# Kernel tuning notes

Measured on AMD Instinct MI355X. Metric: run time of the kernel, lower is better.

Reference implementation:

```python
import jax, jax.numpy as jnp
import numpy as np

N_HEADS = 16
ROPE_BASE = 10000.0


def rope_angles(seq_len, head_dim):
    # freq[n, i] = n / base^(2i/head_dim), shape [N, head_dim//2]
    inv_freq = 1.0 / (ROPE_BASE ** (jnp.arange(0, head_dim, 2, dtype=jnp.float32) / head_dim))
    return jnp.arange(seq_len, dtype=jnp.float32)[:, None] * inv_freq[None, :]


def apply_rope(t, ang):
    # t: [B, h, N, D], ang: [N, D//2]; rotate half-split pairs
    cos = jnp.cos(ang)[None, None]  # [1,1,N,D//2]
    sin = jnp.sin(ang)[None, None]
    d2 = t.shape[-1] // 2
    t1, t2 = t[..., :d2], t[..., d2:]
    return jnp.concatenate([t1 * cos - t2 * sin, t1 * sin + t2 * cos], axis=-1)


def setup_inputs() -> dict:
    key = jax.random.key(0)
    k1, k2, k3 = jax.random.split(key, 3)
    B, N, D = 2, 2048, 2048
    x = jax.random.normal(k1, (B, N, D), dtype=jnp.float32)
    w_qkv = jax.random.normal(k2, (3 * D, D), dtype=jnp.float32) * (D ** -0.5)
    w_proj = jax.random.normal(k3, (D, D), dtype=jnp.float32) * (D ** -0.5)
    b_proj = jnp.zeros((D,), dtype=jnp.float32)
    return {"x": x, "w_qkv": w_qkv, "w_proj": w_proj, "b_proj": b_proj}


def reference(x, w_qkv, w_proj, b_proj):
    B, N, D = x.shape
    h = N_HEADS
    hd = D // h

    qkv = jnp.einsum('bnd,ed->bne', x, w_qkv)  # [B, N, 3D]
    q, k, v = jnp.split(qkv, 3, axis=-1)

    def to_heads(t):  # [B,N,D] -> [B,h,N,hd]
        return t.reshape(B, N, h, hd).transpose(0, 2, 1, 3)

    q, k, v = to_heads(q), to_heads(k), to_heads(v)

    ang = rope_angles(N, hd)
    q = apply_rope(q, ang)
    k = apply_rope(k, ang)

    scale = 1.0 / jnp.sqrt(jnp.asarray(hd, dtype=x.dtype))
    scores = jnp.einsum('bhqd,bhkd->bhqk', q, k) * scale  # [B,h,N,N]
    attn = jax.nn.softmax(scores, axis=-1)
    out = jnp.einsum('bhqk,bhkd->bhqd', attn, v)  # [B,h,N,hd]

    out = out.transpose(0, 2, 1, 3).reshape(B, N, D)
    return jnp.einsum('bnd,ed->bne', out, w_proj) + b_proj
```

## Files before the change

### kernel.cpp

```cpp
#include <hip/hip_runtime.h>
#include <hip/hip_bf16.h>

using bf16 = __hip_bfloat16;
typedef __attribute__((ext_vector_type(8))) short bf16x8;
typedef __attribute__((ext_vector_type(4))) float f32x4;
typedef __attribute__((ext_vector_type(16))) float f32x16;
typedef __attribute__((ext_vector_type(4))) unsigned int u32x4;

constexpr int Bz  = 2;
constexpr int SEQ = 2048;
constexpr int DM  = 2048;
constexpr int H   = 16;
constexpr int HD  = 128;
constexpr long MROWS = (long)Bz * SEQ;
constexpr int EQ  = 3 * DM;
constexpr float QSCALE_L2E = 0.12751743427795914f;

__device__ __forceinline__ float bf2f(bf16 x) { return __bfloat162float(x); }
__device__ __forceinline__ bf16  f2bf(float x) { return __float2bfloat16(x); }

__device__ __forceinline__ float fexp2(float x) {
  float r;
  asm("v_exp_f32 %0, %1" : "=v"(r) : "v"(x));
  return r;
}

template <int N>
__device__ __forceinline__ void waitvm() {
  asm volatile("s_waitcnt vmcnt(%0)" ::"n"(N) : "memory");
}

__device__ __forceinline__ void gl_lds16(const void* g, void* l) {
  __builtin_amdgcn_global_load_lds(
      (const __attribute__((address_space(1))) unsigned int*)g,
      (__attribute__((address_space(3))) unsigned int*)l, 16, 0, 0);
}

__global__ void f32_to_bf16(const float* __restrict__ in, bf16* __restrict__ out, long n) {
  long i = ((long)blockIdx.x * blockDim.x + threadIdx.x) * 4;
  if (i >= n) return;
  float4 v = *(const float4*)(in + i);
  bf16 tmp[4] = {f2bf(v.x), f2bf(v.y), f2bf(v.z), f2bf(v.w)};
  *(uint2*)(out + i) = *(uint2*)tmp;
}

__global__ void rope_table(float* __restrict__ ct, float* __restrict__ st) {
  int idx = blockIdx.x * 256 + threadIdx.x;
  if (idx >= SEQ * 64) return;
  int j = idx & 63, n = idx >> 6;
  double inv = exp(-(double)j / 64.0 * 9.210340371976184);
  double a = (double)n * inv;
  ct[idx] = (float)cos(a);
  st[idx] = (float)sin(a);
}

template <int KTOT, int BN, int NBP, int OUT_BF16>
__global__ __launch_bounds__(512) void gemm128(const bf16* __restrict__ A,
                                               const bf16* __restrict__ Bm,
                                               void* __restrict__ Cv,
                                               const float* __restrict__ bias,
                                               int M, int Nn) {
  constexpr int NT = KTOT / 64;
  __shared__ alignas(16) bf16 lsA[2][128 * 64];
  __shared__ alignas(16) bf16 lsB[2][BN * 64];

  const int nwg = gridDim.x;
  const int f = blockIdx.x;
  const int wg = (f & 7) * (nwg >> 3) + (f >> 3);
  const int nbm = M >> 7;
  const long am0 = (long)(wg % nbm) * 128;
  const long bn0 = (long)(wg / nbm) * BN;

  const int tid = threadIdx.x;
  const int wv = tid >> 6, ln = tid & 63;
  const int wm = wv & 1, wn = wv >> 1;
  const int fr = ln & 15, kq = ln >> 4;
  const int sr8 = ln >> 3;
  const int ss  = ln & 7;

  f32x4 acc[4][2 * NBP] = {};
  bf16x8 af[8];
  bf16x8 bq[4];

  auto stageA = [&](int buf, int t) {
#pragma unroll
    for (int ld = 0; ld < 2; ++ld) {
      const int r = ld * 64 + wv * 8 + sr8;
      const int sl = ss ^ (r & 7);
      gl_lds16(A + (am0 + r) * KTOT + t * 64 + sl * 8, &lsA[buf][(ld * 64 + wv * 8) * 64]);
    }
  };
  auto stageB = [&](int buf, int t, int bp) {
#pragma unroll
    for (int ld = 0; ld < 2; ++ld) {
      const int r = bp * 128 + ld * 64 + wv * 8 + sr8;
      const int sl = ss ^ (r & 7);
      gl_lds16(Bm + (bn0 + r) * KTOT + t * 64 + sl * 8,
               &lsB[buf][(bp * 128 + ld * 64 + wv * 8) * 64]);
    }
  };

  stageA(0, 0);
#pragma unroll
  for (int bp = 0; bp < NBP; ++bp) stageB(0, 0, bp);
  waitvm<0>();
  __builtin_amdgcn_s_barrier();

#pragma unroll 2
  for (int t = 0; t < NT; ++t) {
    const int cur = t & 1;
    const bool pre = (t + 1 < NT);

#pragma unroll
    for (int bp = 0; bp < NBP; ++bp) {
      if (bp == 0) {
#pragma unroll
        for (int i = 0; i < 4; ++i)
#pragma unroll
          for (int ks = 0; ks < 2; ++ks) {
            const int row = (wm + 2 * i) * 16 + fr;
            const int sl = (ks * 4 + kq) ^ (row & 7);
            af[i * 2 + ks] = *(const bf16x8*)((const char*)&lsA[cur][0] + row * 128 + sl * 16);
          }
      }
#pragma unroll
      for (int jj = 0; jj < 2; ++jj)
#pragma unroll
        for (int ks = 0; ks < 2; ++ks) {
          const int row = (wn + 4 * (2 * bp + jj)) * 16 + fr;
          const int sl = (ks * 4 + kq) ^ (row & 7);
          bq[jj * 2 + ks] = *(const bf16x8*)((const char*)&lsB[cur][0] + row * 128 + sl * 16);
        }

      if (pre) {
        if (bp == 0) {
          stageA(cur ^ 1, t + 1);
          stageB(cur ^ 1, t + 1, 0);
          waitvm<2 * NBP>();
        } else if (bp == NBP - 1) {
          stageB(cur ^ 1, t + 1, bp);
          waitvm<2 * (NBP - 1)>();
        } else {
          stageB(cur ^ 1, t + 1, bp);
          waitvm<2 * NBP>();
        }
      } else {
        if (bp == 0) waitvm<(NBP > 2) ? 2 : 0>();
        else waitvm<0>();
      }
      __builtin_amdgcn_s_barrier();

      __builtin_amdgcn_s_setprio(1);
#pragma unroll
      for (int i = 0; i < 4; ++i)
#pragma unroll
        for (int jj = 0; jj < 2; ++jj)
#pragma unroll
          for (int ks = 0; ks < 2; ++ks)
            acc[i][2 * bp + jj] = __builtin_amdgcn_mfma_f32_16x16x32_bf16(
                af[i * 2 + ks], bq[jj * 2 + ks], acc[i][2 * bp + jj], 0, 0, 0);
      __builtin_amdgcn_s_setprio(0);
    }
  }

#pragma unroll
  for (int i = 0; i < 4; ++i) {
    const long row0 = am0 + (wm + 2 * i) * 16 + kq * 4;
#pragma unroll
    for (int j = 0; j < 2 * NBP; ++j) {
      const long col = bn0 + (wn + 4 * j) * 16 + fr;
      const float bv = bias ? bias[col] : 0.f;
#pragma unroll
      for (int q = 0; q < 4; ++q) {
        const float v = acc[i][j][q] + bv;
        if (OUT_BF16) ((bf16*)Cv)[(row0 + q) * Nn + col] = f2bf(v);
        else          ((float*)Cv)[(row0 + q) * Nn + col] = v;
      }
    }
  }
}

__global__ void rope_reshape(const bf16* __restrict__ qkv, const float* __restrict__ ct,
                             const float* __restrict__ st, bf16* __restrict__ q_r,
                             bf16* __restrict__ k_r) {
  long idx = (long)blockIdx.x * 256 + threadIdx.x;
  int j = idx & 63;
  int h = (idx >> 6) & 15;
  int n = (idx >> 10) & 2047;
  int b = (int)(idx >> 21);
  long row = (long)b * SEQ + n;
  float c = ct[n * 64 + j], s = st[n * 64 + j];
  long qoff = row * EQ + h * 128 + j;
  float q1 = bf2f(qkv[qoff]),        q2 = bf2f(qkv[qoff + 64]);
  float k1 = bf2f(qkv[qoff + 2048]), k2 = bf2f(qkv[qoff + 2048 + 64]);
  long obase = ((long)(b * 16 + h) * SEQ + n) * HD + j;
  q_r[obase]      = f2bf((q1 * c - q2 * s) * QSCALE_L2E);
  q_r[obase + 64] = f2bf((q1 * s + q2 * c) * QSCALE_L2E);
  k_r[obase]      = f2bf(k1 * c - k2 * s);
  k_r[obase + 64] = f2bf(k1 * s + k2 * c);
}

__global__ __launch_bounds__(256) void v_transpose(const bf16* __restrict__ qkv,
                                                   bf16* __restrict__ v_t) {
  __shared__ bf16 tile[64][65];
  int bh = blockIdx.z;
  int b = bh >> 4, h = bh & 15;
  int n0 = blockIdx.y * 64, d0 = blockIdx.x * 64;
  int t = threadIdx.x;
#pragma unroll
  for (int p = 0; p < 16; ++p) {
    int e = p * 256 + t;
    int dn = e & 63, nn = e >> 6;
    tile[nn][dn] = qkv[(long)(b * SEQ + n0 + nn) * EQ + 2 * DM + h * 128 + d0 + dn];
  }
  __syncthreads();
#pragma unroll
  for (int p = 0; p < 16; ++p) {
    int e = p * 256 + t;
    int nn = e & 63, dd = e >> 6;
    v_t[((long)bh * HD + d0 + dd) * SEQ + n0 + nn] = tile[nn][dd];
  }
}

__global__ __launch_bounds__(256, 2) void attn_fwd(const bf16* __restrict__ q_r,
                                                   const bf16* __restrict__ k_r,
                                                   const bf16* __restrict__ v_t,
                                                   bf16* __restrict__ ao) {
  __shared__ alignas(16) char lds[65536];

  const int flat = blockIdx.y * gridDim.x + blockIdx.x;
  const int bh = (flat & 7) * 4 + ((flat >> 3) >> 4);
  const int qt = (flat >> 3) & 15;
  const int b = bh >> 4, h = bh & 15;

  const int wv = threadIdx.x >> 6, ln = threadIdx.x & 63;
  const int lh = ln >> 5;
  const int lq = ln & 31;
  const int q0 = qt * 128 + wv * 32;

  bf16x8 aq[8];
  {
    const char* qbase = (const char*)(q_r + ((long)bh * SEQ + q0 + lq) * HD);
#pragma unroll
    for (int ks = 0; ks < 8; ++ks)
      aq[ks] = *(const bf16x8*)(qbase + ks * 32 + lh * 16);
  }

  f32x16 oacc[4] = {};
  float mrow = -1e30f, lsum = 0.f;

  auto stage = [&](int buf, int t) {
    char* kb = lds + buf * 16384;
    char* vb = lds + 32768 + buf * 16384;
#pragma unroll
    for (int cc = 0; cc < 8; ++cc) {
      const int chunk = wv * 8 + cc;
      if (chunk < 16) {
        const int r = chunk * 4 + (ln >> 4);
        const char* src = (const char*)k_r + ((long)bh * SEQ + t * 64 + r) * 256 +
                          (((ln & 15) ^ (r & 15)) << 4);
        gl_lds16(src, kb + chunk * 1024);
      } else {
        const int c2 = chunk - 16;
        const int r = c2 * 8 + (ln >> 3);
        const char* src = (const char*)v_t + ((long)bh * HD + r) * (SEQ * 2) + t * 128 +
                          (((ln & 7) ^ (r & 7)) << 4);
        gl_lds16(src, vb + c2 * 1024);
      }
    }
  };

  stage(0, 0);
  __syncthreads();

  for (int t = 0; t < SEQ / 64; ++t) {
    const int cur = t & 1;
    if (t + 1 < SEQ / 64) stage(cur ^ 1, t + 1);
    const char* kb = lds + cur * 16384;
    const char* vb = lds + 32768 + cur * 16384;

    f32x16 sacc[2] = {};
    __builtin_amdgcn_s_setprio(1);
#pragma unroll
    for (int kvs = 0; kvs < 2; ++kvs) {
      const int kv = kvs * 32 + lq;
#pragma unroll
      for (int ks = 0; ks < 8; ++ks) {
        bf16x8 kf = *(const bf16x8*)(kb + kv * 256 + ((((ks << 1) | lh) ^ (kv & 15)) << 4));
        sacc[kvs] = __builtin_amdgcn_mfma_f32_32x32x16_bf16(kf, aq[ks], sacc[kvs], 0, 0, 0);
      }
    }
    __builtin_amdgcn_s_setprio(0);

    float mx = sacc[0][0];
#pragma unroll
    for (int r = 1; r < 16; ++r) mx = fmaxf(mx, sacc[0][r]);
#pragma unroll
    for (int r = 0; r < 16; ++r) mx = fmaxf(mx, sacc[1][r]);
    mx = fmaxf(mx, __shfl_xor(mx, 32, 64));
    const float mn = fmaxf(mrow, mx);
    const float scale = fexp2(mrow - mn);
    mrow = mn;
    float psum = 0.f;
#pragma unroll
    for (int k2 = 0; k2 < 2; ++k2)
#pragma unroll
      for (int r = 0; r < 16; ++r) {
        const float pv = fexp2(sacc[k2][r] - mn);
        sacc[k2][r] = pv;
        psum += pv;
      }
    psum += __shfl_xor(psum, 32, 64);
    lsum = lsum * scale + psum;
#pragma unroll
    for (int dt = 0; dt < 4; ++dt) oacc[dt] *= scale;

    bf16x8 pfrag[4];
#pragma unroll
    for (int k2 = 0; k2 < 2; ++k2) {
      unsigned int pk[8];
#pragma unroll
      for (int i = 0; i < 8; ++i) {
        unsigned int lo = __bfloat16_as_ushort(f2bf(sacc[k2][2 * i]));
        unsigned int hi = __bfloat16_as_ushort(f2bf(sacc[k2][2 * i + 1]));
        pk[i] = lo | (hi << 16);
      }
#pragma unroll
      for (int fb = 0; fb < 2; ++fb) {
        const unsigned int a0 = pk[fb * 4 + 0], a1 = pk[fb * 4 + 1];
        const unsigned int b0 = pk[fb * 4 + 2], b1 = pk[fb * 4 + 3];
        const unsigned int sb0 = __shfl_xor(b0, 32, 64);
        const unsigned int sb1 = __shfl_xor(b1, 32, 64);
        const unsigned int sa0 = __shfl_xor(a0, 32, 64);
        const unsigned int sa1 = __shfl_xor(a1, 32, 64);
        u32x4 wvec;
        wvec.x = lh ? sb0 : a0;
        wvec.y = lh ? sb1 : a1;
        wvec.z = lh ? b0 : sa0;
        wvec.w = lh ? b1 : sa1;
        pfrag[k2 * 2 + fb] = __builtin_bit_cast(bf16x8, wvec);
      }
    }

    __builtin_amdgcn_s_setprio(1);
#pragma unroll
    for (int dt = 0; dt < 4; ++dt) {
      const int d = dt * 32 + lq;
#pragma unroll
      for (int kk = 0; kk < 4; ++kk) {
        bf16x8 vf = *(const bf16x8*)(vb + d * 128 + ((((kk << 1) | lh) ^ (d & 7)) << 4));
        oacc[dt] = __builtin_amdgcn_mfma_f32_32x32x16_bf16(vf, pfrag[kk], oacc[dt], 0, 0, 0);
      }
    }
    __builtin_amdgcn_s_setprio(0);
    __syncthreads();
  }

  const float inv = 1.0f / lsum;
  bf16* ob = (bf16*)lds;
  const int qloc = wv * 32 + lq;
#pragma unroll
  for (int dt = 0; dt < 4; ++dt)
#pragma unroll
    for (int r = 0; r < 16; ++r) {
      const int d = dt * 32 + (r & 3) + 8 * (r >> 2) + 4 * lh;
      ob[qloc * 132 + d] = f2bf(oacc[dt][r] * inv);
    }
#pragma unroll
  for (int it = 0; it < 8; ++it) {
    const int c = it * 64 + ln;
    const int qq = c >> 4, dc = c & 15;
    const char* srcp = (const char*)ob + (wv * 32 + qq) * 264 + dc * 16;
    uint2 v0 = *(const uint2*)srcp;
    uint2 v1 = *(const uint2*)(srcp + 8);
    uint4 outv;
    outv.x = v0.x; outv.y = v0.y; outv.z = v1.x; outv.w = v1.y;
    *(uint4*)((char*)(ao + ((long)b * SEQ + qt * 128 + wv * 32 + qq) * DM + h * 128) + dc * 16) = outv;
  }
}

extern "C" void kernel_launch(void* const* d_in, const int* in_sizes, int n_in,
                              void* d_out, int out_size, void* d_ws, size_t ws_size,
                              hipStream_t stream) {
  const float* x      = (const float*)d_in[0];
  const float* w_qkv  = (const float*)d_in[1];
  const float* w_proj = (const float*)d_in[2];
  const float* b_proj = (const float*)d_in[3];

  char* ws = (char*)d_ws;
  size_t off = 0;
  auto alloc = [&](size_t bytes) {
    void* p = ws + off;
    off += (bytes + 255) & ~(size_t)255;
    return p;
  };
  bf16* xb     = (bf16*)alloc((size_t)MROWS * DM * 2);
  bf16* wqkvb  = (bf16*)alloc((size_t)EQ * DM * 2);
  bf16* wprojb = (bf16*)alloc((size_t)DM * DM * 2);
  bf16* qkvb   = (bf16*)alloc((size_t)MROWS * EQ * 2);
  bf16* q_r    = (bf16*)alloc((size_t)Bz * H * SEQ * HD * 2);
  bf16* k_r    = (bf16*)alloc((size_t)Bz * H * SEQ * HD * 2);
  bf16* v_t    = (bf16*)alloc((size_t)Bz * H * SEQ * HD * 2);
  bf16* aob    = (bf16*)alloc((size_t)MROWS * DM * 2);
  float* ct    = (float*)alloc((size_t)SEQ * 64 * 4);
  float* st    = (float*)alloc((size_t)SEQ * 64 * 4);

  {
    long n = MROWS * DM;
    f32_to_bf16<<<(int)((n / 4 + 255) / 256), 256, 0, stream>>>(x, xb, n);
  }
  {
    long n = (long)EQ * DM;
    f32_to_bf16<<<(int)((n / 4 + 255) / 256), 256, 0, stream>>>(w_qkv, wqkvb, n);
  }
  {
    long n = (long)DM * DM;
    f32_to_bf16<<<(int)((n / 4 + 255) / 256), 256, 0, stream>>>(w_proj, wprojb, n);
  }
  rope_table<<<(SEQ * 64) / 256, 256, 0, stream>>>(ct, st);

  gemm128<2048, 384, 3, 1><<<(int)(MROWS / 128) * (EQ / 384), 512, 0, stream>>>(
      xb, wqkvb, qkvb, nullptr, (int)MROWS, EQ);

  rope_reshape<<<(int)((long)Bz * SEQ * H * 64 / 256), 256, 0, stream>>>(qkvb, ct, st, q_r, k_r);
  v_transpose<<<dim3(HD / 64, SEQ / 64, Bz * H), 256, 0, stream>>>(qkvb, v_t);

  attn_fwd<<<dim3(16, Bz * H), 256, 0, stream>>>(q_r, k_r, v_t, aob);

  gemm128<2048, 256, 2, 0><<<(int)(MROWS / 128) * (DM / 256), 512, 0, stream>>>(
      aob, wprojb, d_out, b_proj, (int)MROWS, DM);
}
```

Before: 292.8 us.

## Vectorize rope/transpose, enlarge attention tiles, lazy softmax rescale, simplify GEMM pipeline

Rope and V-transpose now move data with 16-byte vector loads and stores instead of scalar accesses. The attention kernel goes to 512-thread blocks covering 256 queries each, so each K/V tile staged in LDS serves twice as many queries. The online softmax now rescales the running max and accumulators only when the new max exceeds the old one by more than 8 in the log2 domain. The GEMM main loop switches to issuing all next-tile prefetches up front with one wait and barrier per K step, replacing the interleaved per-subtile waits. These changes target memory inefficiency and per-tile overhead, at the cost of more LDS and registers per attention block and less overlap inside the GEMM.

```diff
diff --git a/kernel.cpp b/kernel.cpp
--- a/kernel.cpp
+++ b/kernel.cpp
@@ -18,6 +18,9 @@
 
 __device__ __forceinline__ float bf2f(bf16 x) { return __bfloat162float(x); }
 __device__ __forceinline__ bf16  f2bf(float x) { return __float2bfloat16(x); }
+__device__ __forceinline__ float rawbf(short u) {
+  return __uint_as_float(((unsigned int)(unsigned short)u) << 16);
+}
 
 __device__ __forceinline__ float fexp2(float x) {
   float r;
@@ -79,8 +82,6 @@
   const int ss  = ln & 7;
 
   f32x4 acc[4][2 * NBP] = {};
-  bf16x8 af[8];
-  bf16x8 bq[4];
 
   auto stageA = [&](int buf, int t) {
 #pragma unroll
@@ -106,23 +107,27 @@
   waitvm<0>();
   __builtin_amdgcn_s_barrier();
 
-#pragma unroll 2
   for (int t = 0; t < NT; ++t) {
     const int cur = t & 1;
-    const bool pre = (t + 1 < NT);
+    if (t + 1 < NT) {
+      stageA(cur ^ 1, t + 1);
+#pragma unroll
+      for (int bp = 0; bp < NBP; ++bp) stageB(cur ^ 1, t + 1, bp);
+    }
+
+    bf16x8 af[8];
+#pragma unroll
+    for (int i = 0; i < 4; ++i)
+#pragma unroll
+      for (int ks = 0; ks < 2; ++ks) {
+        const int row = (wm + 2 * i) * 16 + fr;
+        const int sl = (ks * 4 + kq) ^ (row & 7);
+        af[i * 2 + ks] = *(const bf16x8*)((const char*)&lsA[cur][0] + row * 128 + sl * 16);
+      }
 
 #pragma unroll
     for (int bp = 0; bp < NBP; ++bp) {
-      if (bp == 0) {
-#pragma unroll
-        for (int i = 0; i < 4; ++i)
-#pragma unroll
-          for (int ks = 0; ks < 2; ++ks) {
-            const int row = (wm + 2 * i) * 16 + fr;
-            const int sl = (ks * 4 + kq) ^ (row & 7);
-            af[i * 2 + ks] = *(const bf16x8*)((const char*)&lsA[cur][0] + row * 128 + sl * 16);
-          }
-      }
+      bf16x8 bq[4];
 #pragma unroll
       for (int jj = 0; jj < 2; ++jj)
 #pragma unroll
@@ -131,25 +136,6 @@
           const int sl = (ks * 4 + kq) ^ (row & 7);
           bq[jj * 2 + ks] = *(const bf16x8*)((const char*)&lsB[cur][0] + row * 128 + sl * 16);
         }
-
-      if (pre) {
-        if (bp == 0) {
-          stageA(cur ^ 1, t + 1);
-          stageB(cur ^ 1, t + 1, 0);
-          waitvm<2 * NBP>();
-        } else if (bp == NBP - 1) {
-          stageB(cur ^ 1, t + 1, bp);
-          waitvm<2 * (NBP - 1)>();
-        } else {
-          stageB(cur ^ 1, t + 1, bp);
-          waitvm<2 * NBP>();
-        }
-      } else {
-        if (bp == 0) waitvm<(NBP > 2) ? 2 : 0>();
-        else waitvm<0>();
-      }
-      __builtin_amdgcn_s_barrier();
-
       __builtin_amdgcn_s_setprio(1);
 #pragma unroll
       for (int i = 0; i < 4; ++i)
@@ -161,6 +147,9 @@
                 af[i * 2 + ks], bq[jj * 2 + ks], acc[i][2 * bp + jj], 0, 0, 0);
       __builtin_amdgcn_s_setprio(0);
     }
+
+    waitvm<0>();
+    __builtin_amdgcn_s_barrier();
   }
 
 #pragma unroll
@@ -184,59 +173,82 @@
                              const float* __restrict__ st, bf16* __restrict__ q_r,
                              bf16* __restrict__ k_r) {
   long idx = (long)blockIdx.x * 256 + threadIdx.x;
-  int j = idx & 63;
-  int h = (idx >> 6) & 15;
-  int n = (idx >> 10) & 2047;
-  int b = (int)(idx >> 21);
+  int j8 = (idx & 7) * 8;
+  int h = (idx >> 3) & 15;
+  int n = (idx >> 7) & 2047;
+  int b = (int)(idx >> 18);
   long row = (long)b * SEQ + n;
-  float c = ct[n * 64 + j], s = st[n * 64 + j];
-  long qoff = row * EQ + h * 128 + j;
-  float q1 = bf2f(qkv[qoff]),        q2 = bf2f(qkv[qoff + 64]);
-  float k1 = bf2f(qkv[qoff + 2048]), k2 = bf2f(qkv[qoff + 2048 + 64]);
-  long obase = ((long)(b * 16 + h) * SEQ + n) * HD + j;
-  q_r[obase]      = f2bf((q1 * c - q2 * s) * QSCALE_L2E);
-  q_r[obase + 64] = f2bf((q1 * s + q2 * c) * QSCALE_L2E);
-  k_r[obase]      = f2bf(k1 * c - k2 * s);
-  k_r[obase + 64] = f2bf(k1 * s + k2 * c);
+  long qoff = row * EQ + h * 128 + j8;
+  bf16x8 q1v = *(const bf16x8*)(qkv + qoff);
+  bf16x8 q2v = *(const bf16x8*)(qkv + qoff + 64);
+  bf16x8 k1v = *(const bf16x8*)(qkv + qoff + 2048);
+  bf16x8 k2v = *(const bf16x8*)(qkv + qoff + 2048 + 64);
+  float4 ca = *(const float4*)(ct + n * 64 + j8);
+  float4 cb = *(const float4*)(ct + n * 64 + j8 + 4);
+  float4 sa = *(const float4*)(st + n * 64 + j8);
+  float4 sb = *(const float4*)(st + n * 64 + j8 + 4);
+  float c[8] = {ca.x, ca.y, ca.z, ca.w, cb.x, cb.y, cb.z, cb.w};
+  float s[8] = {sa.x, sa.y, sa.z, sa.w, sb.x, sb.y, sb.z, sb.w};
+  bf16x8 oq1, oq2, ok1, ok2;
+#pragma unroll
+  for (int m = 0; m < 8; ++m) {
+    float q1 = rawbf(q1v[m]), q2 = rawbf(q2v[m]);
+    float k1 = rawbf(k1v[m]), k2 = rawbf(k2v[m]);
+    oq1[m] = (short)__bfloat16_as_ushort(f2bf((q1 * c[m] - q2 * s[m]) * QSCALE_L2E));
+    oq2[m] = (short)__bfloat16_as_ushort(f2bf((q1 * s[m] + q2 * c[m]) * QSCALE_L2E));
+    ok1[m] = (short)__bfloat16_as_ushort(f2bf(k1 * c[m] - k2 * s[m]));
+    ok2[m] = (short)__bfloat16_as_ushort(f2bf(k1 * s[m] + k2 * c[m]));
+  }
+  long obase = ((long)(b * 16 + h) * SEQ + n) * HD + j8;
+  *(bf16x8*)(q_r + obase)      = oq1;
+  *(bf16x8*)(q_r + obase + 64) = oq2;
+  *(bf16x8*)(k_r + obase)      = ok1;
+  *(bf16x8*)(k_r + obase + 64) = ok2;
 }
 
 __global__ __launch_bounds__(256) void v_transpose(const bf16* __restrict__ qkv,
                                                    bf16* __restrict__ v_t) {
-  __shared__ bf16 tile[64][65];
+  __shared__ bf16 tile[64][72];
   int bh = blockIdx.z;
   int b = bh >> 4, h = bh & 15;
   int n0 = blockIdx.y * 64, d0 = blockIdx.x * 64;
   int t = threadIdx.x;
 #pragma unroll
-  for (int p = 0; p < 16; ++p) {
-    int e = p * 256 + t;
-    int dn = e & 63, nn = e >> 6;
-    tile[nn][dn] = qkv[(long)(b * SEQ + n0 + nn) * EQ + 2 * DM + h * 128 + d0 + dn];
+  for (int it = 0; it < 2; ++it) {
+    int e = it * 256 + t;
+    int nn = e >> 3, dn8 = (e & 7) * 8;
+    bf16x8 v = *(const bf16x8*)(qkv + (long)(b * SEQ + n0 + nn) * EQ + 2 * DM + h * 128 + d0 + dn8);
+#pragma unroll
+    for (int m = 0; m < 8; ++m) tile[nn][dn8 + m] = __ushort_as_bfloat16((unsigned short)v[m]);
   }
   __syncthreads();
 #pragma unroll
-  for (int p = 0; p < 16; ++p) {
-    int e = p * 256 + t;
-    int nn = e & 63, dd = e >> 6;
-    v_t[((long)bh * HD + d0 + dd) * SEQ + n0 + nn] = tile[nn][dd];
-  }
-}
-
-__global__ __launch_bounds__(256, 2) void attn_fwd(const bf16* __restrict__ q_r,
+  for (int it = 0; it < 2; ++it) {
+    int e = it * 256 + t;
+    int dd = e >> 3, nn8 = (e & 7) * 8;
+    bf16x8 o;
+#pragma unroll
+    for (int m = 0; m < 8; ++m)
+      o[m] = (short)__bfloat16_as_ushort(tile[nn8 + m][dd]);
+    *(bf16x8*)(v_t + ((long)bh * HD + d0 + dd) * SEQ + n0 + nn8) = o;
+  }
+}
+
+__global__ __launch_bounds__(512, 2) void attn_fwd(const bf16* __restrict__ q_r,
                                                    const bf16* __restrict__ k_r,
                                                    const bf16* __restrict__ v_t,
                                                    bf16* __restrict__ ao) {
-  __shared__ alignas(16) char lds[65536];
-
-  const int flat = blockIdx.y * gridDim.x + blockIdx.x;
-  const int bh = (flat & 7) * 4 + ((flat >> 3) >> 4);
-  const int qt = (flat >> 3) & 15;
+  __shared__ alignas(16) char lds[69632];
+
+  const int flat = blockIdx.x;
+  const int bh = (flat & 7) * 4 + (flat >> 6);
+  const int qt = (flat >> 3) & 7;
   const int b = bh >> 4, h = bh & 15;
 
   const int wv = threadIdx.x >> 6, ln = threadIdx.x & 63;
   const int lh = ln >> 5;
   const int lq = ln & 31;
-  const int q0 = qt * 128 + wv * 32;
+  const int q0 = qt * 256 + wv * 32;
 
   bf16x8 aq[8];
   {
@@ -253,8 +265,8 @@
     char* kb = lds + buf * 16384;
     char* vb = lds + 32768 + buf * 16384;
 #pragma unroll
-    for (int cc = 0; cc < 8; ++cc) {
-      const int chunk = wv * 8 + cc;
+    for (int cc = 0; cc < 4; ++cc) {
+      const int chunk = wv * 4 + cc;
       if (chunk < 16) {
         const int r = chunk * 4 + (ln >> 4);
         const char* src = (const char*)k_r + ((long)bh * SEQ + t * 64 + r) * 256 +
@@ -298,22 +310,26 @@
 #pragma unroll
     for (int r = 0; r < 16; ++r) mx = fmaxf(mx, sacc[1][r]);
     mx = fmaxf(mx, __shfl_xor(mx, 32, 64));
-    const float mn = fmaxf(mrow, mx);
-    const float scale = fexp2(mrow - mn);
-    mrow = mn;
+
+    if (!__all(mx - mrow <= 8.0f)) {
+      const float mn = fmaxf(mrow, mx);
+      const float scale = fexp2(mrow - mn);
+      mrow = mn;
+      lsum *= scale;
+#pragma unroll
+      for (int dt = 0; dt < 4; ++dt) oacc[dt] *= scale;
+    }
     float psum = 0.f;
 #pragma unroll
     for (int k2 = 0; k2 < 2; ++k2)
 #pragma unroll
       for (int r = 0; r < 16; ++r) {
-        const float pv = fexp2(sacc[k2][r] - mn);
+        const float pv = fexp2(sacc[k2][r] - mrow);
         sacc[k2][r] = pv;
         psum += pv;
       }
     psum += __shfl_xor(psum, 32, 64);
-    lsum = lsum * scale + psum;
-#pragma unroll
-    for (int dt = 0; dt < 4; ++dt) oacc[dt] *= scale;
+    lsum += psum;
 
     bf16x8 pfrag[4];
 #pragma unroll
@@ -375,7 +391,7 @@
     uint2 v1 = *(const uint2*)(srcp + 8);
     uint4 outv;
     outv.x = v0.x; outv.y = v0.y; outv.z = v1.x; outv.w = v1.y;
-    *(uint4*)((char*)(ao + ((long)b * SEQ + qt * 128 + wv * 32 + qq) * DM + h * 128) + dc * 16) = outv;
+    *(uint4*)((char*)(ao + ((long)b * SEQ + qt * 256 + wv * 32 + qq) * DM + h * 128) + dc * 16) = outv;
   }
 }
 
@@ -422,10 +438,10 @@
   gemm128<2048, 384, 3, 1><<<(int)(MROWS / 128) * (EQ / 384), 512, 0, stream>>>(
       xb, wqkvb, qkvb, nullptr, (int)MROWS, EQ);
 
-  rope_reshape<<<(int)((long)Bz * SEQ * H * 64 / 256), 256, 0, stream>>>(qkvb, ct, st, q_r, k_r);
+  rope_reshape<<<(int)((long)Bz * SEQ * H * 8 / 256), 256, 0, stream>>>(qkvb, ct, st, q_r, k_r);
   v_transpose<<<dim3(HD / 64, SEQ / 64, Bz * H), 256, 0, stream>>>(qkvb, v_t);
 
-  attn_fwd<<<dim3(16, Bz * H), 256, 0, stream>>>(q_r, k_r, v_t, aob);
+  attn_fwd<<<256, 512, 0, stream>>>(q_r, k_r, v_t, aob);
 
   gemm128<2048, 256, 2, 0><<<(int)(MROWS / 128) * (DM / 256), 512, 0, stream>>>(
       aob, wprojb, d_out, b_proj, (int)MROWS, DM);
```

New measurement: 312.9 us. 1.07x slower.

## Fuse RoPE and V transpose into QKV GEMM epilogue, enlarge attention tiles, lazy rescale

Applied to the files above, without the earlier changes.

The QKV GEMM epilogue now stages its tile through shared memory and writes rotated, scaled Q and K plus transposed V directly. This removes the intermediate qkv buffer and the separate rope_reshape and v_transpose kernels. The attention kernel moves to 512 threads per block with 256 query rows per block, halving K/V loads per wave. Online softmax now skips the rescale unless the running max grows by more than 8 (log2 domain), which cuts exp and multiply work but lets unnormalized values grow, so precision could suffer.

```diff
diff --git a/kernel.cpp b/kernel.cpp
--- a/kernel.cpp
+++ b/kernel.cpp
@@ -54,15 +54,23 @@
   st[idx] = (float)sin(a);
 }
 
-template <int KTOT, int BN, int NBP, int OUT_BF16>
+template <int KTOT, int BN, int NBP, int FUSE>
 __global__ __launch_bounds__(512) void gemm128(const bf16* __restrict__ A,
                                                const bf16* __restrict__ Bm,
                                                void* __restrict__ Cv,
                                                const float* __restrict__ bias,
+                                               bf16* __restrict__ q_r,
+                                               bf16* __restrict__ k_r,
+                                               bf16* __restrict__ v_t,
+                                               const float* __restrict__ ct,
+                                               const float* __restrict__ st,
                                                int M, int Nn) {
   constexpr int NT = KTOT / 64;
-  __shared__ alignas(16) bf16 lsA[2][128 * 64];
-  __shared__ alignas(16) bf16 lsB[2][BN * 64];
+  constexpr int ASZ = 128 * 64;
+  constexpr int BSZ = BN * 64;
+  __shared__ alignas(16) char smem[2 * ASZ * 2 + 2 * BSZ * 2];
+  bf16* lsA = (bf16*)smem;
+  bf16* lsB = (bf16*)(smem + 2 * ASZ * 2);
 
   const int nwg = gridDim.x;
   const int f = blockIdx.x;
@@ -79,15 +87,13 @@
   const int ss  = ln & 7;
 
   f32x4 acc[4][2 * NBP] = {};
-  bf16x8 af[8];
-  bf16x8 bq[4];
 
   auto stageA = [&](int buf, int t) {
 #pragma unroll
     for (int ld = 0; ld < 2; ++ld) {
       const int r = ld * 64 + wv * 8 + sr8;
       const int sl = ss ^ (r & 7);
-      gl_lds16(A + (am0 + r) * KTOT + t * 64 + sl * 8, &lsA[buf][(ld * 64 + wv * 8) * 64]);
+      gl_lds16(A + (am0 + r) * KTOT + t * 64 + sl * 8, lsA + buf * ASZ + (ld * 64 + wv * 8) * 64);
     }
   };
   auto stageB = [&](int buf, int t, int bp) {
@@ -96,7 +102,7 @@
       const int r = bp * 128 + ld * 64 + wv * 8 + sr8;
       const int sl = ss ^ (r & 7);
       gl_lds16(Bm + (bn0 + r) * KTOT + t * 64 + sl * 8,
-               &lsB[buf][(bp * 128 + ld * 64 + wv * 8) * 64]);
+               lsB + buf * BSZ + (bp * 128 + ld * 64 + wv * 8) * 64);
     }
   };
 
@@ -111,6 +117,7 @@
     const int cur = t & 1;
     const bool pre = (t + 1 < NT);
 
+    bf16x8 af[8];
 #pragma unroll
     for (int bp = 0; bp < NBP; ++bp) {
       if (bp == 0) {
@@ -120,16 +127,19 @@
           for (int ks = 0; ks < 2; ++ks) {
             const int row = (wm + 2 * i) * 16 + fr;
             const int sl = (ks * 4 + kq) ^ (row & 7);
-            af[i * 2 + ks] = *(const bf16x8*)((const char*)&lsA[cur][0] + row * 128 + sl * 16);
+            af[i * 2 + ks] =
+                *(const bf16x8*)((const char*)(lsA + cur * ASZ) + row * 128 + sl * 16);
           }
       }
+      bf16x8 bq[4];
 #pragma unroll
       for (int jj = 0; jj < 2; ++jj)
 #pragma unroll
         for (int ks = 0; ks < 2; ++ks) {
           const int row = (wn + 4 * (2 * bp + jj)) * 16 + fr;
           const int sl = (ks * 4 + kq) ^ (row & 7);
-          bq[jj * 2 + ks] = *(const bf16x8*)((const char*)&lsB[cur][0] + row * 128 + sl * 16);
+          bq[jj * 2 + ks] =
+              *(const bf16x8*)((const char*)(lsB + cur * BSZ) + row * 128 + sl * 16);
         }
 
       if (pre) {
@@ -163,80 +173,86 @@
     }
   }
 
-#pragma unroll
-  for (int i = 0; i < 4; ++i) {
-    const long row0 = am0 + (wm + 2 * i) * 16 + kq * 4;
-#pragma unroll
-    for (int j = 0; j < 2 * NBP; ++j) {
-      const long col = bn0 + (wn + 4 * j) * 16 + fr;
-      const float bv = bias ? bias[col] : 0.f;
-#pragma unroll
-      for (int q = 0; q < 4; ++q) {
-        const float v = acc[i][j][q] + bv;
-        if (OUT_BF16) ((bf16*)Cv)[(row0 + q) * Nn + col] = f2bf(v);
-        else          ((float*)Cv)[(row0 + q) * Nn + col] = v;
-      }
-    }
-  }
-}
-
-__global__ void rope_reshape(const bf16* __restrict__ qkv, const float* __restrict__ ct,
-                             const float* __restrict__ st, bf16* __restrict__ q_r,
-                             bf16* __restrict__ k_r) {
-  long idx = (long)blockIdx.x * 256 + threadIdx.x;
-  int j = idx & 63;
-  int h = (idx >> 6) & 15;
-  int n = (idx >> 10) & 2047;
-  int b = (int)(idx >> 21);
-  long row = (long)b * SEQ + n;
-  float c = ct[n * 64 + j], s = st[n * 64 + j];
-  long qoff = row * EQ + h * 128 + j;
-  float q1 = bf2f(qkv[qoff]),        q2 = bf2f(qkv[qoff + 64]);
-  float k1 = bf2f(qkv[qoff + 2048]), k2 = bf2f(qkv[qoff + 2048 + 64]);
-  long obase = ((long)(b * 16 + h) * SEQ + n) * HD + j;
-  q_r[obase]      = f2bf((q1 * c - q2 * s) * QSCALE_L2E);
-  q_r[obase + 64] = f2bf((q1 * s + q2 * c) * QSCALE_L2E);
-  k_r[obase]      = f2bf(k1 * c - k2 * s);
-  k_r[obase + 64] = f2bf(k1 * s + k2 * c);
-}
-
-__global__ __launch_bounds__(256) void v_transpose(const bf16* __restrict__ qkv,
-                                                   bf16* __restrict__ v_t) {
-  __shared__ bf16 tile[64][65];
-  int bh = blockIdx.z;
-  int b = bh >> 4, h = bh & 15;
-  int n0 = blockIdx.y * 64, d0 = blockIdx.x * 64;
-  int t = threadIdx.x;
-#pragma unroll
-  for (int p = 0; p < 16; ++p) {
-    int e = p * 256 + t;
-    int dn = e & 63, nn = e >> 6;
-    tile[nn][dn] = qkv[(long)(b * SEQ + n0 + nn) * EQ + 2 * DM + h * 128 + d0 + dn];
-  }
-  __syncthreads();
-#pragma unroll
-  for (int p = 0; p < 16; ++p) {
-    int e = p * 256 + t;
-    int nn = e & 63, dd = e >> 6;
-    v_t[((long)bh * HD + d0 + dd) * SEQ + n0 + nn] = tile[nn][dd];
-  }
-}
-
-__global__ __launch_bounds__(256, 2) void attn_fwd(const bf16* __restrict__ q_r,
+  if constexpr (FUSE) {
+    static_assert(BN == 384, "fused epilogue assumes 3 head segments per tile");
+    bf16* eb = (bf16*)smem;
+    __syncthreads();
+#pragma unroll
+    for (int i = 0; i < 4; ++i) {
+      const int r0 = (wm + 2 * i) * 16 + kq * 4;
+#pragma unroll
+      for (int j = 0; j < 2 * NBP; ++j) {
+        const int c = (wn + 4 * j) * 16 + fr;
+        bf16 t4[4];
+#pragma unroll
+        for (int q = 0; q < 4; ++q) t4[q] = f2bf(acc[i][j][q]);
+        *(uint2*)(eb + c * 136 + r0) = *(uint2*)t4;
+      }
+    }
+    __syncthreads();
+    const int bb = (int)(am0 >> 11);
+    const int nbase = (int)(am0 & 2047);
+#pragma unroll
+    for (int cb = 0; cb < 3; ++cb) {
+      const int gc = (int)bn0 + cb * 128;
+      const int seg = gc >> 11;
+      const long bh = bb * 16 + ((gc & 2047) >> 7);
+      if (seg < 2) {
+        bf16* dst = (seg == 0) ? q_r : k_r;
+        const float qs = (seg == 0) ? QSCALE_L2E : 1.0f;
+        for (int itx = 0; itx < 16; ++itx) {
+          const int idx = itx * 512 + tid;
+          const int r = idx >> 6, j = idx & 63;
+          const int n = nbase + r;
+          const float v1 = bf2f(eb[(cb * 128 + j) * 136 + r]);
+          const float v2 = bf2f(eb[(cb * 128 + j + 64) * 136 + r]);
+          const float cc = ct[n * 64 + j], sv = st[n * 64 + j];
+          const long ob = (bh * SEQ + n) * HD + j;
+          dst[ob]      = f2bf((v1 * cc - v2 * sv) * qs);
+          dst[ob + 64] = f2bf((v1 * sv + v2 * cc) * qs);
+        }
+      } else {
+        for (int itx = 0; itx < 4; ++itx) {
+          const int idx = itx * 512 + tid;
+          const int d = idx >> 4, n8 = (idx & 15) * 8;
+          bf16x8 v = *(const bf16x8*)(eb + (cb * 128 + d) * 136 + n8);
+          *(bf16x8*)(v_t + (bh * HD + d) * SEQ + nbase + n8) = v;
+        }
+      }
+    }
+  } else {
+#pragma unroll
+    for (int i = 0; i < 4; ++i) {
+      const long row0 = am0 + (wm + 2 * i) * 16 + kq * 4;
+#pragma unroll
+      for (int j = 0; j < 2 * NBP; ++j) {
+        const long col = bn0 + (wn + 4 * j) * 16 + fr;
+        const float bv = bias ? bias[col] : 0.f;
+#pragma unroll
+        for (int q = 0; q < 4; ++q) {
+          const float v = acc[i][j][q] + bv;
+          ((float*)Cv)[(row0 + q) * Nn + col] = v;
+        }
+      }
+    }
+  }
+}
+
+__global__ __launch_bounds__(512, 2) void attn_fwd(const bf16* __restrict__ q_r,
                                                    const bf16* __restrict__ k_r,
                                                    const bf16* __restrict__ v_t,
                                                    bf16* __restrict__ ao) {
-  __shared__ alignas(16) char lds[65536];
-
-  const int flat = blockIdx.y * gridDim.x + blockIdx.x;
-  const int bh = (flat & 7) * 4 + ((flat >> 3) >> 4);
-  const int qt = (flat >> 3) & 15;
+  __shared__ alignas(16) char lds[69632];
+
+  const int flat = blockIdx.x;
+  const int bh = (flat & 7) * 4 + (flat >> 6);
+  const int qt = (flat >> 3) & 7;
   const int b = bh >> 4, h = bh & 15;
 
   const int wv = threadIdx.x >> 6, ln = threadIdx.x & 63;
   const int lh = ln >> 5;
   const int lq = ln & 31;
-  const int q0 = qt * 128 + wv * 32;
+  const int q0 = qt * 256 + wv * 32;
 
   bf16x8 aq[8];
   {
@@ -253,8 +269,8 @@
     char* kb = lds + buf * 16384;
     char* vb = lds + 32768 + buf * 16384;
 #pragma unroll
-    for (int cc = 0; cc < 8; ++cc) {
-      const int chunk = wv * 8 + cc;
+    for (int cc = 0; cc < 4; ++cc) {
+      const int chunk = wv * 4 + cc;
       if (chunk < 16) {
         const int r = chunk * 4 + (ln >> 4);
         const char* src = (const char*)k_r + ((long)bh * SEQ + t * 64 + r) * 256 +
@@ -298,22 +314,26 @@
 #pragma unroll
     for (int r = 0; r < 16; ++r) mx = fmaxf(mx, sacc[1][r]);
     mx = fmaxf(mx, __shfl_xor(mx, 32, 64));
-    const float mn = fmaxf(mrow, mx);
-    const float scale = fexp2(mrow - mn);
-    mrow = mn;
+
+    if (!__all(mx - mrow <= 8.0f)) {
+      const float mn = fmaxf(mrow, mx);
+      const float scale = fexp2(mrow - mn);
+      mrow = mn;
+      lsum *= scale;
+#pragma unroll
+      for (int dt = 0; dt < 4; ++dt) oacc[dt] *= scale;
+    }
     float psum = 0.f;
 #pragma unroll
     for (int k2 = 0; k2 < 2; ++k2)
 #pragma unroll
       for (int r = 0; r < 16; ++r) {
-        const float pv = fexp2(sacc[k2][r] - mn);
+        const float pv = fexp2(sacc[k2][r] - mrow);
         sacc[k2][r] = pv;
         psum += pv;
       }
     psum += __shfl_xor(psum, 32, 64);
-    lsum = lsum * scale + psum;
-#pragma unroll
-    for (int dt = 0; dt < 4; ++dt) oacc[dt] *= scale;
+    lsum += psum;
 
     bf16x8 pfrag[4];
 #pragma unroll
@@ -375,7 +395,7 @@
     uint2 v1 = *(const uint2*)(srcp + 8);
     uint4 outv;
     outv.x = v0.x; outv.y = v0.y; outv.z = v1.x; outv.w = v1.y;
-    *(uint4*)((char*)(ao + ((long)b * SEQ + qt * 128 + wv * 32 + qq) * DM + h * 128) + dc * 16) = outv;
+    *(uint4*)((char*)(ao + ((long)b * SEQ + qt * 256 + wv * 32 + qq) * DM + h * 128) + dc * 16) = outv;
   }
 }
 
@@ -397,7 +417,6 @@
   bf16* xb     = (bf16*)alloc((size_t)MROWS * DM * 2);
   bf16* wqkvb  = (bf16*)alloc((size_t)EQ * DM * 2);
   bf16* wprojb = (bf16*)alloc((size_t)DM * DM * 2);
-  bf16* qkvb   = (bf16*)alloc((size_t)MROWS * EQ * 2);
   bf16* q_r    = (bf16*)alloc((size_t)Bz * H * SEQ * HD * 2);
   bf16* k_r    = (bf16*)alloc((size_t)Bz * H * SEQ * HD * 2);
   bf16* v_t    = (bf16*)alloc((size_t)Bz * H * SEQ * HD * 2);
@@ -420,13 +439,11 @@
   rope_table<<<(SEQ * 64) / 256, 256, 0, stream>>>(ct, st);
 
   gemm128<2048, 384, 3, 1><<<(int)(MROWS / 128) * (EQ / 384), 512, 0, stream>>>(
-      xb, wqkvb, qkvb, nullptr, (int)MROWS, EQ);
-
-  rope_reshape<<<(int)((long)Bz * SEQ * H * 64 / 256), 256, 0, stream>>>(qkvb, ct, st, q_r, k_r);
-  v_transpose<<<dim3(HD / 64, SEQ / 64, Bz * H), 256, 0, stream>>>(qkvb, v_t);
-
-  attn_fwd<<<dim3(16, Bz * H), 256, 0, stream>>>(q_r, k_r, v_t, aob);
+      xb, wqkvb, nullptr, nullptr, q_r, k_r, v_t, ct, st, (int)MROWS, EQ);
+
+  attn_fwd<<<256, 512, 0, stream>>>(q_r, k_r, v_t, aob);
 
   gemm128<2048, 256, 2, 0><<<(int)(MROWS / 128) * (DM / 256), 512, 0, stream>>>(
-      aob, wprojb, d_out, b_proj, (int)MROWS, DM);
-}
+      aob, wprojb, d_out, b_proj, nullptr, nullptr, nullptr, nullptr, nullptr,
+      (int)MROWS, DM);
+}
```

Measured after the change: 238.4 us. 1.23x faster.
